# Optimization experiments

Measured on AMD Instinct MI355X. Metric: run time of the kernel, lower is better.

The kernel has to match this reference:

```python
import jax, jax.numpy as jnp
import numpy as np
import math

B, L, D, H = 4, 2048, 1024, 16
HD = D // H


def setup_inputs() -> dict:
    key = jax.random.key(0)
    k1, k2, k3 = jax.random.split(key, 3)
    x = jax.random.normal(k1, (B, L, D), dtype=jnp.float32)
    # Linear weights stored as [in, out] so y = x @ W (equivalent to torch x @ W.T)
    Wqkv = jax.random.normal(k2, (D, 3 * D), dtype=jnp.float32) * (1.0 / math.sqrt(D))
    Wproj = jax.random.normal(k3, (D, D), dtype=jnp.float32) * (1.0 / math.sqrt(D))
    attn_mask = jnp.tril(jnp.ones((L, L), dtype=bool))  # True = attend (causal)
    key_padding_mask = jnp.zeros((B, L), dtype=bool)     # True = padded (none here)
    return {"x": x, "Wqkv": Wqkv, "Wproj": Wproj,
            "attn_mask": attn_mask, "key_padding_mask": key_padding_mask}


def reference(x, Wqkv, Wproj, attn_mask, key_padding_mask):
    Bx, Lx, Dx = x.shape
    qkv = x @ Wqkv                              # [B, L, 3D]
    q, k, v = jnp.split(qkv, 3, axis=-1)
    def shape(t):
        return t.reshape(Bx, Lx, H, HD).transpose(0, 2, 1, 3)  # [B, H, L, hd]
    q, k, v = shape(q), shape(k), shape(v)
    att = jnp.einsum('bhqd,bhkd->bhqk', q, k) / math.sqrt(HD)  # [B, H, L, L]
    neg_inf = jnp.float32(-jnp.inf)
    att = jnp.where(attn_mask[None, None, :, :], att, neg_inf)
    att = jnp.where(key_padding_mask[:, None, None, :], neg_inf, att)
    att = jax.nn.softmax(att, axis=-1)
    y = jnp.einsum('bhqk,bhkd->bhqd', att, v)   # [B, H, L, hd]
    y = y.transpose(0, 2, 1, 3).reshape(Bx, Lx, Dx)
    return y @ Wproj
```

## Files before the change

kernel.cpp:

```cpp
#include <hip/hip_runtime.h>
#include <cstdint>
#include <cstddef>


typedef __attribute__((ext_vector_type(8))) __bf16 bf16x8;
typedef __attribute__((ext_vector_type(4))) __bf16 bf16x4;
typedef __attribute__((ext_vector_type(4))) float f32x4;
typedef __attribute__((ext_vector_type(16))) float f32x16;

__device__ __forceinline__ f32x4 mfma_bf16(bf16x8 a, bf16x8 b, f32x4 c) {
  return __builtin_amdgcn_mfma_f32_16x16x32_bf16(a, b, c, 0, 0, 0);
}

__device__ __forceinline__ f32x16 mfma32(bf16x8 a, bf16x8 b, f32x16 c) {
  return __builtin_amdgcn_mfma_f32_32x32x16_bf16(a, b, c, 0, 0, 0);
}

__device__ __forceinline__ unsigned cvtpk(float a, float b) {
  unsigned r;
  asm("v_cvt_pk_bf16_f32 %0, %1, %2" : "=v"(r) : "v"(a), "v"(b));
  return r;
}

__device__ __forceinline__ void async_copy16(const void* gsrc, void* ldsdst) {
  __builtin_amdgcn_global_load_lds(
      (const __attribute__((address_space(1))) void*)gsrc,
      (__attribute__((address_space(3))) void*)ldsdst, 16, 0, 0);
}

__global__ __launch_bounds__(256) void f32_to_bf16(
    const float* __restrict__ in, __bf16* __restrict__ out) {
  const size_t i = ((size_t)blockIdx.x * 256 + threadIdx.x) * 4;
  const float4 v = *(const float4*)&in[i];
  bf16x4 o = {(__bf16)v.x, (__bf16)v.y, (__bf16)v.z, (__bf16)v.w};
  *(bf16x4*)&out[i] = o;
}

__global__ __launch_bounds__(256) void transpose_f32_bf16(
    const float* __restrict__ in, __bf16* __restrict__ out, int R, int C) {
  __shared__ float tile[32][33];
  const int c0 = blockIdx.x * 32;
  const int r0 = blockIdx.y * 32;
  const int tx = threadIdx.x & 31;
  const int ty = threadIdx.x >> 5;
#pragma unroll
  for (int i = 0; i < 32; i += 8)
    tile[ty + i][tx] = in[(size_t)(r0 + ty + i) * C + c0 + tx];
  __syncthreads();
#pragma unroll
  for (int i = 0; i < 32; i += 8)
    out[(size_t)(c0 + ty + i) * R + r0 + tx] = (__bf16)tile[tx][ty + i];
}


__global__ __launch_bounds__(256) void gemm_bt_f32out(
    const __bf16* __restrict__ A, const __bf16* __restrict__ BT,
    float* __restrict__ C, int M, int N, int K) {
  __shared__ __bf16 As[128 * 32];
  __shared__ __bf16 Bs[128 * 32];
  const int tid = threadIdx.x;
  const int wave = tid >> 6;
  const int lane = tid & 63;
  const int n16 = lane & 15;
  const int quad = lane >> 4;
  const int m0 = blockIdx.x * 128;
  const int n0 = blockIdx.y * 128;
  const int wr = wave >> 1;
  const int wc = wave & 1;

  const f32x4 zero = {0.f, 0.f, 0.f, 0.f};
  f32x4 acc[4][4];
#pragma unroll
  for (int i = 0; i < 4; ++i)
#pragma unroll
    for (int j = 0; j < 4; ++j) acc[i][j] = zero;

  const int KT = K >> 5;
  for (int kt = 0; kt < KT; ++kt) {
    const int k0 = kt << 5;
#pragma unroll
    for (int r = 0; r < 2; ++r) {
      const int li = (r << 8) + tid;
      const int row = li >> 2;
      const int kp8 = (li & 3) << 3;
      const int lbase = ((r << 8) + (wave << 6)) << 3;
      async_copy16(&A[(size_t)(m0 + row) * K + k0 + kp8], &As[lbase]);
      async_copy16(&BT[(size_t)(n0 + row) * K + k0 + kp8], &Bs[lbase]);
    }
    __syncthreads();
    bf16x8 af[4], bf[4];
#pragma unroll
    for (int t = 0; t < 4; ++t) {
      af[t] = *(const bf16x8*)&As[(wr * 64 + t * 16 + n16) * 32 + quad * 8];
      bf[t] = *(const bf16x8*)&Bs[(wc * 64 + t * 16 + n16) * 32 + quad * 8];
    }
#pragma unroll
    for (int mt = 0; mt < 4; ++mt)
#pragma unroll
      for (int nt = 0; nt < 4; ++nt)
        acc[mt][nt] = mfma_bf16(af[mt], bf[nt], acc[mt][nt]);
    __syncthreads();
  }
#pragma unroll
  for (int mt = 0; mt < 4; ++mt) {
#pragma unroll
    for (int r = 0; r < 4; ++r) {
      const int m = m0 + wr * 64 + mt * 16 + quad * 4 + r;
#pragma unroll
      for (int nt = 0; nt < 4; ++nt) {
        const int n = n0 + wc * 64 + nt * 16 + n16;
        C[(size_t)m * N + n] = acc[mt][nt][r];
      }
    }
  }
}

__global__ __launch_bounds__(256) void gemm_qkv(
    const __bf16* __restrict__ A, const __bf16* __restrict__ BT,
    __bf16* __restrict__ Q, __bf16* __restrict__ Kh, __bf16* __restrict__ VT) {
  __shared__ __bf16 As[128 * 32];
  __shared__ __bf16 Bs[128 * 32];
  const int tid = threadIdx.x;
  const int wave = tid >> 6;
  const int lane = tid & 63;
  const int n16 = lane & 15;
  const int quad = lane >> 4;
  const int m0 = blockIdx.x * 128;
  const int n0 = blockIdx.y * 128;
  const int wr = wave >> 1;
  const int wc = wave & 1;
  const int K = 1024;

  const f32x4 zero = {0.f, 0.f, 0.f, 0.f};
  f32x4 acc[4][4];
#pragma unroll
  for (int i = 0; i < 4; ++i)
#pragma unroll
    for (int j = 0; j < 4; ++j) acc[i][j] = zero;

  for (int kt = 0; kt < 32; ++kt) {
    const int k0 = kt << 5;
#pragma unroll
    for (int r = 0; r < 2; ++r) {
      const int li = (r << 8) + tid;
      const int row = li >> 2;
      const int kp8 = (li & 3) << 3;
      const int lbase = ((r << 8) + (wave << 6)) << 3;
      async_copy16(&A[(size_t)(m0 + row) * K + k0 + kp8], &As[lbase]);
      async_copy16(&BT[(size_t)(n0 + row) * K + k0 + kp8], &Bs[lbase]);
    }
    __syncthreads();
    bf16x8 af[4], bf[4];
#pragma unroll
    for (int t = 0; t < 4; ++t) {
      af[t] = *(const bf16x8*)&As[(wr * 64 + t * 16 + n16) * 32 + quad * 8];
      bf[t] = *(const bf16x8*)&Bs[(wc * 64 + t * 16 + n16) * 32 + quad * 8];
    }
#pragma unroll
    for (int mt = 0; mt < 4; ++mt)
#pragma unroll
      for (int nt = 0; nt < 4; ++nt)
        acc[mt][nt] = mfma_bf16(af[mt], bf[nt], acc[mt][nt]);
    __syncthreads();
  }

  __syncthreads();
  const int b = m0 >> 11;
  __bf16* tw = (wave < 2 ? As : Bs) + (wave & 1) * 2048;
  const int l0w = (m0 & 2047) + wr * 64;

  if (n0 < 2048) {
    const float QSCALE = 0.125f * 1.44269504089f;
    const bool isQ = (n0 < 1024);
    const int h = ((n0 & 1023) >> 6) + wc;
    __bf16* dst = isQ ? Q : Kh;
    const size_t base = ((size_t)(b * 16 + h) * 2048) * 64;
#pragma unroll
    for (int pass = 0; pass < 2; ++pass) {
#pragma unroll
      for (int mt = 2 * pass; mt < 2 * pass + 2; ++mt) {
#pragma unroll
        for (int nt = 0; nt < 4; ++nt)
#pragma unroll
          for (int r = 0; r < 4; ++r) {
            const int hd = nt * 16 + n16;
            const int mm = (mt & 1) * 16 + quad * 4 + r;
            const float v =
                isQ ? acc[mt][nt][r] * QSCALE : acc[mt][nt][r];
            tw[mm * 64 + (((hd >> 3) ^ (mm & 7)) << 3) + (hd & 7)] =
                (__bf16)v;
          }
      }
#pragma unroll
      for (int i = 0; i < 4; ++i) {
        const int c = lane + 64 * i;
        const int row = c >> 3;
        const int hd0 = (c & 7) << 3;
        const int phys = (c & 7) ^ (row & 7);
        const bf16x8 v = *(const bf16x8*)&tw[row * 64 + phys * 8];
        *(bf16x8*)&dst[base + (size_t)(l0w + pass * 32 + row) * 64 + hd0] = v;
      }
    }
  } else {
    const int h = ((n0 - 2048) >> 6) + wc;
    const size_t bhead = (size_t)(b * 16 + h);
#pragma unroll
    for (int pass = 0; pass < 2; ++pass) {
#pragma unroll
      for (int nt = 2 * pass; nt < 2 * pass + 2; ++nt) {
#pragma unroll
        for (int mt = 0; mt < 4; ++mt)
#pragma unroll
          for (int r = 0; r < 4; ++r) {
            const int hdp = (nt & 1) * 16 + n16;
            const int mm = mt * 16 + quad * 4 + r;
            const int phys = (mm >> 3) ^ (hdp & 7);
            tw[hdp * 64 + phys * 8 + (mm & 7)] = (__bf16)acc[mt][nt][r];
          }
      }
#pragma unroll
      for (int i = 0; i < 4; ++i) {
        const int c = lane + 64 * i;
        const int row = c >> 3;
        const int phys = (c & 7) ^ (row & 7);
        const bf16x8 v = *(const bf16x8*)&tw[row * 64 + phys * 8];
        *(bf16x8*)&VT[(bhead * 64 + pass * 32 + row) * 2048 + l0w +
                      (c & 7) * 8] = v;
      }
    }
  }
}

__global__ __launch_bounds__(256, 2) void flash_attn(
    const __bf16* __restrict__ Q, const __bf16* __restrict__ Kh,
    const __bf16* __restrict__ VT, __bf16* __restrict__ Y) {
  __shared__ __bf16 Ks[2][64 * 64];
  __shared__ __bf16 Vs[2][64 * 64];
  const int bh = blockIdx.x;
  const int p = blockIdx.y;
  const int tid = threadIdx.x;
  const int wave = tid >> 6;
  const int lane = tid & 63;
  const int lrow = lane & 31;
  const int hi = lane >> 5;
  const int lswz = lane & 7;
  const __bf16* Qb = Q + (size_t)bh * 2048 * 64;
  const __bf16* Kb = Kh + (size_t)bh * 2048 * 64;
  const __bf16* Vb = VT + (size_t)bh * 64 * 2048;
  const int b = bh >> 4;
  const int h = bh & 15;
  const f32x16 zero16 = {0.f, 0.f, 0.f, 0.f, 0.f, 0.f, 0.f, 0.f,
                         0.f, 0.f, 0.f, 0.f, 0.f, 0.f, 0.f, 0.f};

  const int srow = tid >> 3;
  const int sswz = ((tid & 7) ^ (srow & 7)) << 3;
  const size_t kg0 = (size_t)srow * 64 + sswz;
  const size_t kg1 = (size_t)(srow + 32) * 64 + sswz;
  const size_t vg0 = (size_t)srow * 2048 + sswz;
  const size_t vg1 = (size_t)(srow + 32) * 2048 + sswz;
  const int ldst0 = wave * 512;
  const int ldst1 = 2048 + wave * 512;

#pragma unroll
  for (int tt = 0; tt < 2; ++tt) {
    const int t = tt ? 15 - p : p;
    const int q0w = t * 128 + wave * 32;
    const int myq = q0w + lrow;

    bf16x8 qf[4];
#pragma unroll
    for (int i = 0; i < 4; ++i)
      qf[i] = *(const bf16x8*)&Qb[(size_t)myq * 64 + i * 16 + hi * 8];

    f32x16 o0 = zero16, o1 = zero16;
    float lsum = 0.f;
    const int nsteps = 2 * (t + 1);

    __syncthreads();
    async_copy16(&Kb[kg0], &Ks[0][ldst0]);
    async_copy16(&Kb[kg1], &Ks[0][ldst1]);
    async_copy16(&Vb[vg0], &Vs[0][ldst0]);
    async_copy16(&Vb[vg1], &Vs[0][ldst1]);

    for (int kt = 0; kt < nsteps; ++kt) {
      const int buf = kt & 1;
      const int c0 = kt << 6;
      __syncthreads();
      if (kt + 1 < nsteps) {
        const int nb = buf ^ 1;
        const int cn = c0 + 64;
        async_copy16(&Kb[kg0 + (size_t)cn * 64], &Ks[nb][ldst0]);
        async_copy16(&Kb[kg1 + (size_t)cn * 64], &Ks[nb][ldst1]);
        async_copy16(&Vb[vg0 + cn], &Vs[nb][ldst0]);
        async_copy16(&Vb[vg1 + cn], &Vs[nb][ldst1]);
      }
      if (c0 > q0w + 31) continue;

      const __bf16* ks = Ks[buf];
      const __bf16* vs = Vs[buf];

      f32x16 sc[2];
#pragma unroll
      for (int ch = 0; ch < 2; ++ch) {
        sc[ch] = zero16;
#pragma unroll
        for (int i = 0; i < 4; ++i) {
          const bf16x8 kf = *(const bf16x8*)&ks[(ch * 32 + lrow) * 64 +
                                                (((2 * i + hi) ^ lswz) << 3)];
          sc[ch] = mfma32(kf, qf[i], sc[ch]);
        }
      }
      if (c0 + 63 > q0w) {
#pragma unroll
        for (int ch = 0; ch < 2; ++ch)
#pragma unroll
          for (int r = 0; r < 16; ++r) {
            const int k = c0 + ch * 32 + (r & 3) + 8 * (r >> 2) + 4 * hi;
            float e = __builtin_amdgcn_exp2f(sc[ch][r]);
            e = (k <= myq) ? e : 0.f;
            sc[ch][r] = e;
            lsum += e;
          }
      } else {
#pragma unroll
        for (int ch = 0; ch < 2; ++ch)
#pragma unroll
          for (int r = 0; r < 16; ++r) {
            const float e = __builtin_amdgcn_exp2f(sc[ch][r]);
            sc[ch][r] = e;
            lsum += e;
          }
      }
#pragma unroll
      for (int ch = 0; ch < 2; ++ch) {
#pragma unroll
        for (int kc = 0; kc < 2; ++kc) {
          unsigned c01 = cvtpk(sc[ch][kc * 8 + 0], sc[ch][kc * 8 + 1]);
          unsigned c23 = cvtpk(sc[ch][kc * 8 + 2], sc[ch][kc * 8 + 3]);
          unsigned c45 = cvtpk(sc[ch][kc * 8 + 4], sc[ch][kc * 8 + 5]);
          unsigned c67 = cvtpk(sc[ch][kc * 8 + 6], sc[ch][kc * 8 + 7]);
          asm("v_permlane32_swap_b32 %0, %1" : "+v"(c01), "+v"(c45));
          asm("v_permlane32_swap_b32 %0, %1" : "+v"(c23), "+v"(c67));
          union {
            unsigned u[4];
            bf16x8 v;
          } pu;
          pu.u[0] = c01;
          pu.u[1] = c23;
          pu.u[2] = c45;
          pu.u[3] = c67;
          const int kch = ch * 4 + kc * 2 + hi;
          {
            const bf16x8 vf0 = *(const bf16x8*)&vs[(0 * 32 + lrow) * 64 +
                                                   ((kch ^ lswz) << 3)];
            o0 = mfma32(pu.v, vf0, o0);
            const bf16x8 vf1 = *(const bf16x8*)&vs[(1 * 32 + lrow) * 64 +
                                                   ((kch ^ lswz) << 3)];
            o1 = mfma32(pu.v, vf1, o1);
          }
        }
      }
    }

    lsum += __shfl_xor(lsum, 32);
    const float inv = 1.0f / lsum;
    float invr[16];
#pragma unroll
    for (int r = 0; r < 16; ++r)
      invr[r] = __shfl(inv, (r & 3) + 8 * (r >> 2) + 4 * hi);
#pragma unroll
    for (int r = 0; r < 16; ++r) {
      const int row = q0w + (r & 3) + 8 * (r >> 2) + 4 * hi;
      const size_t yb = (size_t)(b * 2048 + row) * 1024 + h * 64;
      Y[yb + lrow] = (__bf16)(o0[r] * invr[r]);
      Y[yb + 32 + lrow] = (__bf16)(o1[r] * invr[r]);
    }
  }
}

extern "C" void kernel_launch(void* const* d_in, const int* in_sizes, int n_in,
                              void* d_out, int out_size, void* d_ws,
                              size_t ws_size, hipStream_t stream) {
  const float* x = (const float*)d_in[0];
  const float* Wqkv = (const float*)d_in[1];
  const float* Wproj = (const float*)d_in[2];
  float* out = (float*)d_out;

  char* ws = (char*)d_ws;
  __bf16* xb = (__bf16*)ws;     ws += (size_t)8192 * 1024 * 2;
  __bf16* WqkvT = (__bf16*)ws;  ws += (size_t)3072 * 1024 * 2;
  __bf16* WprojT = (__bf16*)ws; ws += (size_t)1024 * 1024 * 2;
  __bf16* Qs = (__bf16*)ws;     ws += (size_t)64 * 2048 * 64 * 2;
  __bf16* Ks = (__bf16*)ws;     ws += (size_t)64 * 2048 * 64 * 2;
  __bf16* VTs = (__bf16*)ws;    ws += (size_t)64 * 64 * 2048 * 2;
  __bf16* attn = xb;

  f32_to_bf16<<<8192, 256, 0, stream>>>(x, xb);
  transpose_f32_bf16<<<dim3(96, 32), 256, 0, stream>>>(Wqkv, WqkvT, 1024, 3072);
  transpose_f32_bf16<<<dim3(32, 32), 256, 0, stream>>>(Wproj, WprojT, 1024, 1024);
  gemm_qkv<<<dim3(64, 24), 256, 0, stream>>>(xb, WqkvT, Qs, Ks, VTs);
  flash_attn<<<dim3(64, 8), 256, 0, stream>>>(Qs, Ks, VTs, attn);
  gemm_bt_f32out<<<dim3(64, 8), 256, 0, stream>>>(attn, WprojT, out,
                                                  8192, 1024, 1024);
}
```

Measured before the change: 247.0 us.

## Rewrite QKV GEMM with 256x256 tiles, double-buffered swizzled LDS, and XCD-aware remap

The QKV projection GEMM moves from 128x128 tiles with 4 waves and single-buffered 32-wide K steps to 256x256 tiles with 8 waves and 64-wide K steps. It double-buffers A/B in 128KB of dynamic LDS with an XOR swizzle and issues the next tile's async loads before computing the current one. It also raises MFMA priority inside barrier-fenced compute phases and remaps block IDs so each chiplet handles contiguous tiles. The aim is more data reuse per load, global latency hidden behind compute, and fewer bank conflicts, at the cost of heavy register and LDS use and 384 blocks that may underfill the GPU.

After: 253.1 us. 1.02x slower.

```diff
diff --git a/kernel.cpp b/kernel.cpp
--- a/kernel.cpp
+++ b/kernel.cpp
@@ -51,7 +51,6 @@
   for (int i = 0; i < 32; i += 8)
     out[(size_t)(c0 + ty + i) * R + r0 + tx] = (__bf16)tile[tx][ty + i];
 }
-
 
 __global__ __launch_bounds__(256) void gemm_bt_f32out(
     const __bf16* __restrict__ A, const __bf16* __restrict__ BT,
@@ -115,78 +114,120 @@
   }
 }
 
-__global__ __launch_bounds__(256) void gemm_qkv(
+__global__ __launch_bounds__(512, 2) void gemm_qkv(
     const __bf16* __restrict__ A, const __bf16* __restrict__ BT,
     __bf16* __restrict__ Q, __bf16* __restrict__ Kh, __bf16* __restrict__ VT) {
-  __shared__ __bf16 As[128 * 32];
-  __shared__ __bf16 Bs[128 * 32];
+  extern __shared__ __bf16 smem[];
+  const int K = 1024;
+  const int wg = (blockIdx.x & 7) * 48 + (blockIdx.x >> 3);
+  const int bm = wg / 12;
+  const int bn = wg % 12;
+  const int m0 = bm << 8;
+  const int n0 = bn << 8;
+
   const int tid = threadIdx.x;
   const int wave = tid >> 6;
   const int lane = tid & 63;
   const int n16 = lane & 15;
   const int quad = lane >> 4;
-  const int m0 = blockIdx.x * 128;
-  const int n0 = blockIdx.y * 128;
-  const int wr = wave >> 1;
-  const int wc = wave & 1;
-  const int K = 1024;
+  const int wr = wave >> 2;
+  const int wc = wave & 3;
+
+  const int srow = wave * 8 + (lane >> 3);
+  const int schunk = ((lane & 7) ^ ((lane >> 3) & 7)) << 3;
+  const __bf16* aS = &A[(size_t)(m0 + srow) * K + schunk];
+  const __bf16* bS = &BT[(size_t)(n0 + srow) * K + schunk];
+  __bf16* dstW = smem + wave * 512;
 
   const f32x4 zero = {0.f, 0.f, 0.f, 0.f};
-  f32x4 acc[4][4];
-#pragma unroll
-  for (int i = 0; i < 4; ++i)
+  f32x4 acc[8][4];
+#pragma unroll
+  for (int i = 0; i < 8; ++i)
 #pragma unroll
     for (int j = 0; j < 4; ++j) acc[i][j] = zero;
 
-  for (int kt = 0; kt < 32; ++kt) {
-    const int k0 = kt << 5;
-#pragma unroll
-    for (int r = 0; r < 2; ++r) {
-      const int li = (r << 8) + tid;
-      const int row = li >> 2;
-      const int kp8 = (li & 3) << 3;
-      const int lbase = ((r << 8) + (wave << 6)) << 3;
-      async_copy16(&A[(size_t)(m0 + row) * K + k0 + kp8], &As[lbase]);
-      async_copy16(&BT[(size_t)(n0 + row) * K + k0 + kp8], &Bs[lbase]);
-    }
-    __syncthreads();
-    bf16x8 af[4], bf[4];
-#pragma unroll
-    for (int t = 0; t < 4; ++t) {
-      af[t] = *(const bf16x8*)&As[(wr * 64 + t * 16 + n16) * 32 + quad * 8];
-      bf[t] = *(const bf16x8*)&Bs[(wc * 64 + t * 16 + n16) * 32 + quad * 8];
-    }
-#pragma unroll
-    for (int mt = 0; mt < 4; ++mt)
-#pragma unroll
-      for (int nt = 0; nt < 4; ++nt)
-        acc[mt][nt] = mfma_bf16(af[mt], bf[nt], acc[mt][nt]);
-    __syncthreads();
-  }
-
-  __syncthreads();
+#pragma unroll
+  for (int i = 0; i < 4; ++i) {
+    async_copy16(aS + (size_t)i * 65536, dstW + i * 4096);
+    async_copy16(bS + (size_t)i * 65536, dstW + 16384 + i * 4096);
+  }
+
+  for (int t = 0; t < 16; ++t) {
+    const int base = (t & 1) << 15;
+    asm volatile("s_waitcnt vmcnt(0)" ::: "memory");
+    __builtin_amdgcn_s_barrier();
+    if (t + 1 < 16) {
+      const int nbase = ((t + 1) & 1) << 15;
+      const __bf16* aT = aS + (t + 1) * 64;
+      const __bf16* bT = bS + (t + 1) * 64;
+#pragma unroll
+      for (int i = 0; i < 4; ++i) {
+        async_copy16(aT + (size_t)i * 65536, dstW + nbase + i * 4096);
+        async_copy16(bT + (size_t)i * 65536, dstW + nbase + 16384 + i * 4096);
+      }
+    }
+    const __bf16* As = smem + base;
+    const __bf16* Bs = smem + base + 16384;
+    bf16x8 bfr[4][2];
+#pragma unroll
+    for (int g = 0; g < 4; ++g)
+#pragma unroll
+      for (int kk = 0; kk < 2; ++kk) {
+        const int row = wc * 64 + g * 16 + n16;
+        const int phys = ((kk * 4 + quad) ^ (n16 & 7)) << 3;
+        bfr[g][kk] = *(const bf16x8*)&Bs[row * 64 + phys];
+      }
+#pragma unroll
+    for (int q = 0; q < 4; ++q) {
+      bf16x8 afr[2][2];
+#pragma unroll
+      for (int fi = 0; fi < 2; ++fi)
+#pragma unroll
+        for (int kk = 0; kk < 2; ++kk) {
+          const int row = wr * 128 + (2 * q + fi) * 16 + n16;
+          const int phys = ((kk * 4 + quad) ^ (n16 & 7)) << 3;
+          afr[fi][kk] = *(const bf16x8*)&As[row * 64 + phys];
+        }
+      __builtin_amdgcn_s_barrier();
+      asm volatile("s_waitcnt lgkmcnt(0)" ::: "memory");
+      __builtin_amdgcn_sched_barrier(0);
+      __builtin_amdgcn_s_setprio(1);
+#pragma unroll
+      for (int fi = 0; fi < 2; ++fi)
+#pragma unroll
+        for (int g = 0; g < 4; ++g)
+#pragma unroll
+          for (int kk = 0; kk < 2; ++kk)
+            acc[2 * q + fi][g] =
+                mfma_bf16(afr[fi][kk], bfr[g][kk], acc[2 * q + fi][g]);
+      __builtin_amdgcn_s_setprio(0);
+      __builtin_amdgcn_s_barrier();
+    }
+  }
+
+  __bf16* tw = smem + wave * 2048;
   const int b = m0 >> 11;
-  __bf16* tw = (wave < 2 ? As : Bs) + (wave & 1) * 2048;
-  const int l0w = (m0 & 2047) + wr * 64;
-
-  if (n0 < 2048) {
+  const int l0w = (m0 & 2047) + wr * 128;
+  const int n = n0 + wc * 64;
+
+  if (n < 2048) {
     const float QSCALE = 0.125f * 1.44269504089f;
-    const bool isQ = (n0 < 1024);
-    const int h = ((n0 & 1023) >> 6) + wc;
+    const bool isQ = (n < 1024);
+    const int h = (n & 1023) >> 6;
     __bf16* dst = isQ ? Q : Kh;
-    const size_t base = ((size_t)(b * 16 + h) * 2048) * 64;
-#pragma unroll
-    for (int pass = 0; pass < 2; ++pass) {
-#pragma unroll
-      for (int mt = 2 * pass; mt < 2 * pass + 2; ++mt) {
-#pragma unroll
-        for (int nt = 0; nt < 4; ++nt)
+    const size_t bbase = ((size_t)(b * 16 + h) * 2048) * 64;
+#pragma unroll
+    for (int p = 0; p < 4; ++p) {
+#pragma unroll
+      for (int fi = 0; fi < 2; ++fi) {
+        const int f = 2 * p + fi;
+#pragma unroll
+        for (int g = 0; g < 4; ++g)
 #pragma unroll
           for (int r = 0; r < 4; ++r) {
-            const int hd = nt * 16 + n16;
-            const int mm = (mt & 1) * 16 + quad * 4 + r;
-            const float v =
-                isQ ? acc[mt][nt][r] * QSCALE : acc[mt][nt][r];
+            const int hd = g * 16 + n16;
+            const int mm = fi * 16 + quad * 4 + r;
+            const float v = isQ ? acc[f][g][r] * QSCALE : acc[f][g][r];
             tw[mm * 64 + (((hd >> 3) ^ (mm & 7)) << 3) + (hd & 7)] =
                 (__bf16)v;
           }
@@ -198,36 +239,41 @@
         const int hd0 = (c & 7) << 3;
         const int phys = (c & 7) ^ (row & 7);
         const bf16x8 v = *(const bf16x8*)&tw[row * 64 + phys * 8];
-        *(bf16x8*)&dst[base + (size_t)(l0w + pass * 32 + row) * 64 + hd0] = v;
+        *(bf16x8*)&dst[bbase + (size_t)(l0w + p * 32 + row) * 64 + hd0] = v;
       }
     }
   } else {
-    const int h = ((n0 - 2048) >> 6) + wc;
+    const int h = (n - 2048) >> 6;
     const size_t bhead = (size_t)(b * 16 + h);
 #pragma unroll
-    for (int pass = 0; pass < 2; ++pass) {
-#pragma unroll
-      for (int nt = 2 * pass; nt < 2 * pass + 2; ++nt) {
-#pragma unroll
-        for (int mt = 0; mt < 4; ++mt)
-#pragma unroll
-          for (int r = 0; r < 4; ++r) {
-            const int hdp = (nt & 1) * 16 + n16;
-            const int mm = mt * 16 + quad * 4 + r;
-            const int phys = (mm >> 3) ^ (hdp & 7);
-            tw[hdp * 64 + phys * 8 + (mm & 7)] = (__bf16)acc[mt][nt][r];
+    for (int ph = 0; ph < 2; ++ph)
+#pragma unroll
+      for (int lh = 0; lh < 2; ++lh) {
+#pragma unroll
+        for (int gi = 0; gi < 2; ++gi) {
+          const int g = 2 * ph + gi;
+#pragma unroll
+          for (int fi = 0; fi < 4; ++fi) {
+            const int f = 4 * lh + fi;
+#pragma unroll
+            for (int r = 0; r < 4; ++r) {
+              const int hdp = gi * 16 + n16;
+              const int mm = fi * 16 + quad * 4 + r;
+              const int phys = (mm >> 3) ^ (hdp & 7);
+              tw[hdp * 64 + phys * 8 + (mm & 7)] = (__bf16)acc[f][g][r];
+            }
           }
-      }
-#pragma unroll
-      for (int i = 0; i < 4; ++i) {
-        const int c = lane + 64 * i;
-        const int row = c >> 3;
-        const int phys = (c & 7) ^ (row & 7);
-        const bf16x8 v = *(const bf16x8*)&tw[row * 64 + phys * 8];
-        *(bf16x8*)&VT[(bhead * 64 + pass * 32 + row) * 2048 + l0w +
-                      (c & 7) * 8] = v;
-      }
-    }
+        }
+#pragma unroll
+        for (int i = 0; i < 4; ++i) {
+          const int c = lane + 64 * i;
+          const int row = c >> 3;
+          const int phys = (c & 7) ^ (row & 7);
+          const bf16x8 v = *(const bf16x8*)&tw[row * 64 + phys * 8];
+          *(bf16x8*)&VT[(bhead * 64 + ph * 32 + row) * 2048 + l0w + lh * 64 +
+                        (c & 7) * 8] = v;
+        }
+      }
   }
 }
 
@@ -395,10 +441,17 @@
   __bf16* VTs = (__bf16*)ws;    ws += (size_t)64 * 64 * 2048 * 2;
   __bf16* attn = xb;
 
+  static bool attrSet = false;
+  if (!attrSet) {
+    hipFuncSetAttribute((const void*)gemm_qkv,
+                        hipFuncAttributeMaxDynamicSharedMemorySize, 131072);
+    attrSet = true;
+  }
+
   f32_to_bf16<<<8192, 256, 0, stream>>>(x, xb);
   transpose_f32_bf16<<<dim3(96, 32), 256, 0, stream>>>(Wqkv, WqkvT, 1024, 3072);
   transpose_f32_bf16<<<dim3(32, 32), 256, 0, stream>>>(Wproj, WprojT, 1024, 1024);
-  gemm_qkv<<<dim3(64, 24), 256, 0, stream>>>(xb, WqkvT, Qs, Ks, VTs);
+  gemm_qkv<<<384, 512, 131072, stream>>>(xb, WqkvT, Qs, Ks, VTs);
   flash_attn<<<dim3(64, 8), 256, 0, stream>>>(Qs, Ks, VTs, attn);
   gemm_bt_f32out<<<dim3(64, 8), 256, 0, stream>>>(attn, WprojT, out,
                                                   8192, 1024, 1024);
```

## Rewrite QKV and output GEMMs with triple-buffered 128x256 tiles and swizzled LDS

Applied to the files above, without the earlier changes.

Both GEMMs now share one core that uses 512-thread blocks over 128x256 output tiles with a K-step of 64. Operand tiles are triple-buffered in dynamic shared memory and loaded asynchronously two steps ahead, with manual waitcnt and barriers so loads overlap the MFMA work. LDS rows are XOR-swizzled to avoid bank conflicts, MFMA sections get raised priority, and workgroup IDs are remapped for better L2 locality. This targets the load-stall-compute serialization of the old single-buffered 128x128 kernels. The cost is a large shared-memory footprint (147 KB) and hardcoded K=1024 sizes.

New measurement: 239.5 us. 1.03x faster.

```diff
diff --git a/kernel.cpp b/kernel.cpp
--- a/kernel.cpp
+++ b/kernel.cpp
@@ -53,126 +53,84 @@
 }
 
 
-__global__ __launch_bounds__(256) void gemm_bt_f32out(
+#define GEMM128x256_CORE(Aptr, Bptr)                                         \
+  const int srow = tid >> 3;                                      \
+  const int schunk = ((tid & 7) ^ (srow & 7)) << 3;                          \
+  const __bf16* aBase = &(Aptr)[(size_t)(m0 + srow) * 1024 + schunk];        \
+  const __bf16* bBase = &(Bptr)[(size_t)(n0 + srow) * 1024 + schunk];        \
+  auto stgTile = [&](int kt, int b3) {                                       \
+    __bf16* dst = smem + b3 * 24576 + wave * 512;                            \
+    async_copy16(aBase + kt * 64, dst);                                      \
+    async_copy16(aBase + 65536 + kt * 64, dst + 4096);                       \
+    _Pragma("unroll") for (int u = 0; u < 4; ++u)                            \
+        async_copy16(bBase + (size_t)u * 65536 + kt * 64,                    \
+                     dst + 8192 + u * 4096);                                 \
+  };                                                                         \
+  const f32x4 zero = {0.f, 0.f, 0.f, 0.f};                                   \
+  f32x4 acc[4][4];                                                           \
+  _Pragma("unroll") for (int i = 0; i < 4; ++i)                              \
+      _Pragma("unroll") for (int j = 0; j < 4; ++j) acc[i][j] = zero;        \
+  stgTile(0, 0);                                                             \
+  stgTile(1, 1);                                                             \
+  asm volatile("s_waitcnt vmcnt(6)" ::: "memory");      \
+  __builtin_amdgcn_s_barrier();                                              \
+  for (int t = 0; t < 16; ++t) {                                             \
+    const __bf16* As = smem + (t % 3) * 24576;                               \
+    const __bf16* Bs = As + 8192;                                            \
+    bf16x8 af[4][2], bfr[4][2];                                              \
+    _Pragma("unroll") for (int mt = 0; mt < 4; ++mt)                         \
+        _Pragma("unroll") for (int kk = 0; kk < 2; ++kk) af[mt][kk] =        \
+            *(const bf16x8*)&As[(wr * 64 + mt * 16 + n16) * 64 +             \
+                                (((kk * 4 + quad) ^ (n16 & 7)) << 3)];       \
+    _Pragma("unroll") for (int nt = 0; nt < 4; ++nt)                         \
+        _Pragma("unroll") for (int kk = 0; kk < 2; ++kk) bfr[nt][kk] =       \
+            *(const bf16x8*)&Bs[(wc * 64 + nt * 16 + n16) * 64 +             \
+                                (((kk * 4 + quad) ^ (n16 & 7)) << 3)];       \
+    stgTile((t + 2) & 15, (t + 2) % 3);           \
+    __builtin_amdgcn_s_barrier();                                            \
+    asm volatile("s_waitcnt lgkmcnt(0)" ::: "memory");                       \
+    __builtin_amdgcn_sched_barrier(0);                                       \
+    __builtin_amdgcn_s_setprio(1);                                           \
+    _Pragma("unroll") for (int mt = 0; mt < 4; ++mt)                         \
+        _Pragma("unroll") for (int nt = 0; nt < 4; ++nt)                     \
+            _Pragma("unroll") for (int kk = 0; kk < 2; ++kk)                 \
+                acc[mt][nt] = mfma_bf16(af[mt][kk], bfr[nt][kk],             \
+                                        acc[mt][nt]);                        \
+    __builtin_amdgcn_s_setprio(0);                                           \
+    asm volatile("s_waitcnt vmcnt(6)" ::: "memory");     \
+    __builtin_amdgcn_s_barrier();                                            \
+  }                                                                          \
+  asm volatile("s_waitcnt vmcnt(0)" ::: "memory");        \
+  __builtin_amdgcn_s_barrier();
+
+__global__ __launch_bounds__(512, 2) void gemm_qkv(
     const __bf16* __restrict__ A, const __bf16* __restrict__ BT,
-    float* __restrict__ C, int M, int N, int K) {
-  __shared__ __bf16 As[128 * 32];
-  __shared__ __bf16 Bs[128 * 32];
+    __bf16* __restrict__ Q, __bf16* __restrict__ Kh, __bf16* __restrict__ VT) {
+  extern __shared__ __bf16 smem[];
+  const int wg = (blockIdx.x & 7) * 96 + (blockIdx.x >> 3);
+  const int bm = wg / 12;
+  const int bn = wg % 12;
+  const int m0 = bm << 7;
+  const int n0 = bn << 8;
   const int tid = threadIdx.x;
   const int wave = tid >> 6;
   const int lane = tid & 63;
   const int n16 = lane & 15;
   const int quad = lane >> 4;
-  const int m0 = blockIdx.x * 128;
-  const int n0 = blockIdx.y * 128;
-  const int wr = wave >> 1;
-  const int wc = wave & 1;
-
-  const f32x4 zero = {0.f, 0.f, 0.f, 0.f};
-  f32x4 acc[4][4];
-#pragma unroll
-  for (int i = 0; i < 4; ++i)
-#pragma unroll
-    for (int j = 0; j < 4; ++j) acc[i][j] = zero;
-
-  const int KT = K >> 5;
-  for (int kt = 0; kt < KT; ++kt) {
-    const int k0 = kt << 5;
-#pragma unroll
-    for (int r = 0; r < 2; ++r) {
-      const int li = (r << 8) + tid;
-      const int row = li >> 2;
-      const int kp8 = (li & 3) << 3;
-      const int lbase = ((r << 8) + (wave << 6)) << 3;
-      async_copy16(&A[(size_t)(m0 + row) * K + k0 + kp8], &As[lbase]);
-      async_copy16(&BT[(size_t)(n0 + row) * K + k0 + kp8], &Bs[lbase]);
-    }
-    __syncthreads();
-    bf16x8 af[4], bf[4];
-#pragma unroll
-    for (int t = 0; t < 4; ++t) {
-      af[t] = *(const bf16x8*)&As[(wr * 64 + t * 16 + n16) * 32 + quad * 8];
-      bf[t] = *(const bf16x8*)&Bs[(wc * 64 + t * 16 + n16) * 32 + quad * 8];
-    }
-#pragma unroll
-    for (int mt = 0; mt < 4; ++mt)
-#pragma unroll
-      for (int nt = 0; nt < 4; ++nt)
-        acc[mt][nt] = mfma_bf16(af[mt], bf[nt], acc[mt][nt]);
-    __syncthreads();
-  }
-#pragma unroll
-  for (int mt = 0; mt < 4; ++mt) {
-#pragma unroll
-    for (int r = 0; r < 4; ++r) {
-      const int m = m0 + wr * 64 + mt * 16 + quad * 4 + r;
-#pragma unroll
-      for (int nt = 0; nt < 4; ++nt) {
-        const int n = n0 + wc * 64 + nt * 16 + n16;
-        C[(size_t)m * N + n] = acc[mt][nt][r];
-      }
-    }
-  }
-}
-
-__global__ __launch_bounds__(256) void gemm_qkv(
-    const __bf16* __restrict__ A, const __bf16* __restrict__ BT,
-    __bf16* __restrict__ Q, __bf16* __restrict__ Kh, __bf16* __restrict__ VT) {
-  __shared__ __bf16 As[128 * 32];
-  __shared__ __bf16 Bs[128 * 32];
-  const int tid = threadIdx.x;
-  const int wave = tid >> 6;
-  const int lane = tid & 63;
-  const int n16 = lane & 15;
-  const int quad = lane >> 4;
-  const int m0 = blockIdx.x * 128;
-  const int n0 = blockIdx.y * 128;
-  const int wr = wave >> 1;
-  const int wc = wave & 1;
-  const int K = 1024;
-
-  const f32x4 zero = {0.f, 0.f, 0.f, 0.f};
-  f32x4 acc[4][4];
-#pragma unroll
-  for (int i = 0; i < 4; ++i)
-#pragma unroll
-    for (int j = 0; j < 4; ++j) acc[i][j] = zero;
-
-  for (int kt = 0; kt < 32; ++kt) {
-    const int k0 = kt << 5;
-#pragma unroll
-    for (int r = 0; r < 2; ++r) {
-      const int li = (r << 8) + tid;
-      const int row = li >> 2;
-      const int kp8 = (li & 3) << 3;
-      const int lbase = ((r << 8) + (wave << 6)) << 3;
-      async_copy16(&A[(size_t)(m0 + row) * K + k0 + kp8], &As[lbase]);
-      async_copy16(&BT[(size_t)(n0 + row) * K + k0 + kp8], &Bs[lbase]);
-    }
-    __syncthreads();
-    bf16x8 af[4], bf[4];
-#pragma unroll
-    for (int t = 0; t < 4; ++t) {
-      af[t] = *(const bf16x8*)&As[(wr * 64 + t * 16 + n16) * 32 + quad * 8];
-      bf[t] = *(const bf16x8*)&Bs[(wc * 64 + t * 16 + n16) * 32 + quad * 8];
-    }
-#pragma unroll
-    for (int mt = 0; mt < 4; ++mt)
-#pragma unroll
-      for (int nt = 0; nt < 4; ++nt)
-        acc[mt][nt] = mfma_bf16(af[mt], bf[nt], acc[mt][nt]);
-    __syncthreads();
-  }
-
-  __syncthreads();
+  const int wr = wave >> 2;
+  const int wc = wave & 3;
+
+  GEMM128x256_CORE(A, BT)
+
+  __bf16* tw = smem + wave * 2048;
   const int b = m0 >> 11;
-  __bf16* tw = (wave < 2 ? As : Bs) + (wave & 1) * 2048;
   const int l0w = (m0 & 2047) + wr * 64;
-
-  if (n0 < 2048) {
+  const int n = n0 + wc * 64;
+
+  if (n < 2048) {
     const float QSCALE = 0.125f * 1.44269504089f;
-    const bool isQ = (n0 < 1024);
-    const int h = ((n0 & 1023) >> 6) + wc;
+    const bool isQ = (n < 1024);
+    const int h = (n & 1023) >> 6;
     __bf16* dst = isQ ? Q : Kh;
     const size_t base = ((size_t)(b * 16 + h) * 2048) * 64;
 #pragma unroll
@@ -185,8 +143,7 @@
           for (int r = 0; r < 4; ++r) {
             const int hd = nt * 16 + n16;
             const int mm = (mt & 1) * 16 + quad * 4 + r;
-            const float v =
-                isQ ? acc[mt][nt][r] * QSCALE : acc[mt][nt][r];
+            const float v = isQ ? acc[mt][nt][r] * QSCALE : acc[mt][nt][r];
             tw[mm * 64 + (((hd >> 3) ^ (mm & 7)) << 3) + (hd & 7)] =
                 (__bf16)v;
           }
@@ -202,7 +159,7 @@
       }
     }
   } else {
-    const int h = ((n0 - 2048) >> 6) + wc;
+    const int h = (n - 2048) >> 6;
     const size_t bhead = (size_t)(b * 16 + h);
 #pragma unroll
     for (int pass = 0; pass < 2; ++pass) {
@@ -226,6 +183,39 @@
         const bf16x8 v = *(const bf16x8*)&tw[row * 64 + phys * 8];
         *(bf16x8*)&VT[(bhead * 64 + pass * 32 + row) * 2048 + l0w +
                       (c & 7) * 8] = v;
+      }
+    }
+  }
+}
+
+__global__ __launch_bounds__(512, 2) void gemm_bt_f32out(
+    const __bf16* __restrict__ A, const __bf16* __restrict__ BT,
+    float* __restrict__ C) {
+  extern __shared__ __bf16 smem[];
+  const int wg = (blockIdx.x & 7) * 32 + (blockIdx.x >> 3);
+  const int bm = wg >> 2;
+  const int bn = wg & 3;
+  const int m0 = bm << 7;
+  const int n0 = bn << 8;
+  const int tid = threadIdx.x;
+  const int wave = tid >> 6;
+  const int lane = tid & 63;
+  const int n16 = lane & 15;
+  const int quad = lane >> 4;
+  const int wr = wave >> 2;
+  const int wc = wave & 3;
+
+  GEMM128x256_CORE(A, BT)
+
+#pragma unroll
+  for (int mt = 0; mt < 4; ++mt) {
+#pragma unroll
+    for (int r = 0; r < 4; ++r) {
+      const int m = m0 + wr * 64 + mt * 16 + quad * 4 + r;
+#pragma unroll
+      for (int nt = 0; nt < 4; ++nt) {
+        const int nn = n0 + wc * 64 + nt * 16 + n16;
+        C[(size_t)m * 1024 + nn] = acc[mt][nt][r];
       }
     }
   }
@@ -395,11 +385,19 @@
   __bf16* VTs = (__bf16*)ws;    ws += (size_t)64 * 64 * 2048 * 2;
   __bf16* attn = xb;
 
+  static bool attrSet = false;
+  if (!attrSet) {
+    hipFuncSetAttribute((const void*)gemm_qkv,
+                        hipFuncAttributeMaxDynamicSharedMemorySize, 147456);
+    hipFuncSetAttribute((const void*)gemm_bt_f32out,
+                        hipFuncAttributeMaxDynamicSharedMemorySize, 147456);
+    attrSet = true;
+  }
+
   f32_to_bf16<<<8192, 256, 0, stream>>>(x, xb);
   transpose_f32_bf16<<<dim3(96, 32), 256, 0, stream>>>(Wqkv, WqkvT, 1024, 3072);
   transpose_f32_bf16<<<dim3(32, 32), 256, 0, stream>>>(Wproj, WprojT, 1024, 1024);
-  gemm_qkv<<<dim3(64, 24), 256, 0, stream>>>(xb, WqkvT, Qs, Ks, VTs);
+  gemm_qkv<<<768, 512, 147456, stream>>>(xb, WqkvT, Qs, Ks, VTs);
   flash_attn<<<dim3(64, 8), 256, 0, stream>>>(Qs, Ks, VTs, attn);
-  gemm_bt_f32out<<<dim3(64, 8), 256, 0, stream>>>(attn, WprojT, out,
-                                                  8192, 1024, 1024);
-}
+  gemm_bt_f32out<<<256, 512, 147456, stream>>>(attn, WprojT, out);
+}
```
